# Kernel tuning notes

Measured on AMD Instinct MI355X. Metric: run time of the kernel, lower is better.

The kernel has to match this reference:

```python
import jax, jax.numpy as jnp
import numpy as np

N_NODES = 50000
N_EDGES = 800000
N_GRAPHS = 256
W_SCALE = 0.05  # keep activations bounded through 5 relu conv layers


def setup_inputs() -> dict:
    key = jax.random.key(0)
    ks = jax.random.split(key, 16)
    rn = lambda k, shape: W_SCALE * jax.random.normal(k, shape, dtype=jnp.float32)
    return {
        "x": jax.random.normal(ks[0], (N_NODES, 336), dtype=jnp.float32),
        "edge_index": jax.random.randint(ks[1], (2, N_EDGES), 0, N_NODES, dtype=jnp.int32),
        "batch": jnp.sort(jax.random.randint(ks[2], (N_NODES,), 0, N_GRAPHS, dtype=jnp.int32)),
        "w1_rel": rn(ks[3], (100, 336)),
        "w1_root": rn(ks[4], (100, 336)),
        "b1": rn(ks[5], (100,)),
        "w_rel": rn(ks[6], (4, 100, 100)),
        "w_root": rn(ks[7], (4, 100, 100)),
        "b": rn(ks[8], (4, 100)),
        "lw1": rn(ks[9], (100, 100)),
        "lb1": rn(ks[10], (100,)),
        "lw2": rn(ks[11], (100, 100)),
        "lb2": rn(ks[12], (100,)),
        "lw3": rn(ks[13], (29, 100)),
        "lb3": rn(ks[14], (29,)),
    }


def _graph_conv(x, edge_index, w_rel, w_root, bias):
    # PyG GraphConv: out_i = W_rel @ (sum_{j->i} x_j) + b + W_root @ x_i
    src, dst = edge_index[0], edge_index[1]
    agg = jax.ops.segment_sum(x[src], dst, num_segments=x.shape[0])  # [N, d_in]
    return agg @ w_rel.T + bias + x @ w_root.T


def reference(x, edge_index, batch, w1_rel, w1_root, b1, w_rel, w_root, b,
              lw1, lb1, lw2, lb2, lw3, lb3):
    h = jax.nn.relu(_graph_conv(x, edge_index, w1_rel, w1_root, b1))  # [N,100]
    for i in range(4):  # conv2..conv5 (structurally distinct params)
        h = jax.nn.relu(_graph_conv(h, edge_index, w_rel[i], w_root[i], b[i]))
    # global_mean_pool over graphs
    sums = jax.ops.segment_sum(h, batch, num_segments=N_GRAPHS)          # [G,100]
    counts = jax.ops.segment_sum(jnp.ones((h.shape[0],), h.dtype), batch,
                                 num_segments=N_GRAPHS)                  # [G]
    pooled = sums / jnp.maximum(counts, 1.0)[:, None]
    h = jax.nn.relu(pooled @ lw1.T + lb1)
    h = jax.nn.relu(h @ lw2.T + lb2)
    return h @ lw3.T + lb3  # [G, 29]
```

## Files before the change

### kernel.cpp

```cpp
#include <hip/hip_runtime.h>

#define N_NODES 50000
#define N_EDGES 800000
#define N_GRAPHS 256
#define F 100

#define SCAN_B 512
#define SCAN_NB 98
#define SCAN_PAD (SCAN_NB * SCAN_B)

#define PART_SZ 6250
#define FILL_CHUNK 2048

#define SROW 72

typedef __attribute__((ext_vector_type(8))) short bf16x8;
typedef __attribute__((ext_vector_type(4))) float f32x4;
typedef unsigned short ushort_t;
typedef unsigned int uint_t;

__device__ inline ushort_t f2bf(float f) {
  uint_t u = __float_as_uint(f);
  uint_t r = (u + 0x7fffu + ((u >> 16) & 1u)) >> 16;
  return (ushort_t)r;
}


__global__ __launch_bounds__(256) void hist_kernel(const int* __restrict__ dst,
                                                   int* __restrict__ cnt, int E) {
  int part = blockIdx.x & 7;
  int lo = part * PART_SZ, hi = lo + PART_SZ;
  int base = (blockIdx.x >> 3) * FILL_CHUNK;
  int end = base + FILL_CHUNK; if (end > E) end = E;
  for (int i = base + threadIdx.x; i < end; i += 256) {
    int d = dst[i];
    if (d >= lo && d < hi) atomicAdd(&cnt[d], 1);
  }
}

__global__ __launch_bounds__(SCAN_B) void scan1_kernel(const int* __restrict__ cnt,
                                                       int* __restrict__ excl,
                                                       int* __restrict__ bsum) {
  __shared__ int sh[SCAN_B];
  int t = threadIdx.x;
  int i = blockIdx.x * SCAN_B + t;
  int v = cnt[i];
  sh[t] = v;
  __syncthreads();
  for (int off = 1; off < SCAN_B; off <<= 1) {
    int u = (t >= off) ? sh[t - off] : 0;
    __syncthreads();
    sh[t] += u;
    __syncthreads();
  }
  excl[i] = sh[t] - v;
  if (t == SCAN_B - 1) bsum[blockIdx.x] = sh[t];
}

__global__ __launch_bounds__(128) void scan2_kernel(int* __restrict__ bsum) {
  __shared__ int sh[128];
  int t = threadIdx.x;
  int v = (t < SCAN_NB) ? bsum[t] : 0;
  sh[t] = v;
  __syncthreads();
  for (int off = 1; off < 128; off <<= 1) {
    int u = (t >= off) ? sh[t - off] : 0;
    __syncthreads();
    sh[t] += u;
    __syncthreads();
  }
  if (t < SCAN_NB) bsum[t] = sh[t] - v;
}

__global__ __launch_bounds__(SCAN_B) void scan3_kernel(const int* __restrict__ excl,
                                                       const int* __restrict__ bsum,
                                                       int* __restrict__ offs,
                                                       int* __restrict__ cursor) {
  int i = blockIdx.x * SCAN_B + threadIdx.x;
  int v = excl[i] + bsum[blockIdx.x];
  if (i <= N_NODES) { offs[i] = v; cursor[i] = v; }
}

__global__ __launch_bounds__(256) void fill_kernel(const int* __restrict__ src,
                                                   const int* __restrict__ dst,
                                                   int* __restrict__ cursor,
                                                   int* __restrict__ csr_src, int E) {
  int part = blockIdx.x & 7;
  int lo = part * PART_SZ, hi = lo + PART_SZ;
  int base = (blockIdx.x >> 3) * FILL_CHUNK;
  int end = base + FILL_CHUNK; if (end > E) end = E;
  for (int i = base + threadIdx.x; i < end; i += 256) {
    int d = dst[i];
    if (d >= lo && d < hi) {
      int p = atomicAdd(&cursor[d], 1);
      csr_src[p] = src[i];
    }
  }
}


__global__ void pack_w1_kernel(const float* __restrict__ w1_rel, const float* __restrict__ w1_root,
                               ushort_t* __restrict__ Wp1) {
  int row = blockIdx.x;
  for (int k = threadIdx.x; k < 384; k += 128) {
    float v = 0.f;
    if (k < 336) {
      if (row < 100) v = w1_rel[row * 336 + k];
      else if (row < 200) v = w1_root[(row - 100) * 336 + k];
    }
    Wp1[(size_t)row * 384 + k] = f2bf(v);
  }
}

__global__ void pack_w_kernel(const float* __restrict__ w_rel, const float* __restrict__ w_root,
                              ushort_t* __restrict__ Wp) {
  int row = blockIdx.x;
  int l = blockIdx.y;
  int k = threadIdx.x;
  float v = 0.f;
  if (k < 100) {
    if (row < 100) v = w_rel[((size_t)l * 100 + row) * 100 + k];
    else if (row < 200) v = w_root[((size_t)l * 100 + row - 100) * 100 + k];
  }
  Wp[((size_t)l * 208 + row) * 128 + k] = f2bf(v);
}


template <bool AF32>
__global__ __launch_bounds__(256) void conv_mfma(
    const void* __restrict__ Aptr, const ushort_t* __restrict__ Wp,
    const float* __restrict__ bias,
    ushort_t* __restrict__ Zrel, ushort_t* __restrict__ Zroot, int Kp) {
  __shared__ short alds[64 * SROW];
  __shared__ short blds[208 * SROW];
  __shared__ float bias_s[104];

  int tid = threadIdx.x;
  int n0 = blockIdx.x * 64;
  if (tid < 100) bias_s[tid] = bias[tid];

  f32x4 acc[13];
#pragma unroll
  for (int b = 0; b < 13; ++b) acc[b] = (f32x4)0.f;

  int w = tid >> 6, lane = tid & 63, q = lane >> 4, m16 = lane & 15;

  int ar[2], aq[2];
#pragma unroll
  for (int u = 0; u < 2; ++u) { int c = tid + u * 256; ar[u] = c >> 3; aq[u] = c & 7; }

  bf16x8 areg[2], breg[7];

  auto load_chunk = [&](int k0) {
#pragma unroll
    for (int u = 0; u < 2; ++u) {
      int node = n0 + ar[u];
      int k = k0 + aq[u] * 8;
      bf16x8 val = (bf16x8)0;
      if (AF32) {
        if (node < N_NODES && k < 336) {
          const float* p = (const float*)Aptr + (size_t)node * 336 + k;
          float4 f0 = *(const float4*)p;
          float4 f1 = *(const float4*)(p + 4);
          val[0] = (short)f2bf(f0.x); val[1] = (short)f2bf(f0.y);
          val[2] = (short)f2bf(f0.z); val[3] = (short)f2bf(f0.w);
          val[4] = (short)f2bf(f1.x); val[5] = (short)f2bf(f1.y);
          val[6] = (short)f2bf(f1.z); val[7] = (short)f2bf(f1.w);
        }
      } else {
        if (node < N_NODES)
          val = *(const bf16x8*)((const short*)Aptr + (size_t)node * 128 + k);
      }
      areg[u] = val;
    }
#pragma unroll
    for (int u = 0; u < 7; ++u) {
      int c = tid + u * 256;
      if (c < 1664) {
        int r = c >> 3, qq = c & 7;
        breg[u] = *(const bf16x8*)((const short*)Wp + (size_t)r * Kp + k0 + qq * 8);
      }
    }
  };

  load_chunk(0);

  for (int k0 = 0; k0 < Kp; k0 += 64) {
#pragma unroll
    for (int u = 0; u < 2; ++u)
      *(bf16x8*)&alds[ar[u] * SROW + aq[u] * 8] = areg[u];
#pragma unroll
    for (int u = 0; u < 7; ++u) {
      int c = tid + u * 256;
      if (c < 1664) {
        int r = c >> 3, qq = c & 7;
        *(bf16x8*)&blds[r * SROW + qq * 8] = breg[u];
      }
    }
    __syncthreads();
    if (k0 + 64 < Kp) load_chunk(k0 + 64);
#pragma unroll
    for (int s = 0; s < 2; ++s) {
      bf16x8 a = *(const bf16x8*)&alds[(w * 16 + m16) * SROW + s * 32 + q * 8];
#pragma unroll
      for (int b = 0; b < 13; ++b) {
        bf16x8 bf = *(const bf16x8*)&blds[(b * 16 + m16) * SROW + s * 32 + q * 8];
        acc[b] = __builtin_amdgcn_mfma_f32_16x16x32_bf16(a, bf, acc[b], 0, 0, 0);
      }
    }
    __syncthreads();
  }

  int node_base = n0 + w * 16 + q * 4;
#pragma unroll
  for (int b = 0; b < 13; ++b) {
    int n = b * 16 + m16;
#pragma unroll
    for (int r = 0; r < 4; ++r) {
      int node = node_base + r;
      if (node >= N_NODES) continue;
      float v = acc[b][r];
      if (n < 100) {
        Zrel[(size_t)node * 100 + n] = f2bf(v);
      } else if (n < 200) {
        Zroot[(size_t)node * 100 + (n - 100)] = f2bf(v + bias_s[n - 100]);
      }
    }
  }
}


__global__ __launch_bounds__(256) void gather_bf16(
    const ushort_t* __restrict__ Zrel, const ushort_t* __restrict__ Zroot,
    const int* __restrict__ offs, const int* __restrict__ csr,
    ushort_t* __restrict__ H) {
  int node = blockIdx.x * 4 + (threadIdx.x >> 6);
  node = __builtin_amdgcn_readfirstlane(node);
  int lane = threadIdx.x & 63;
  int off = (lane < 50 ? lane : 49) * 2;

  uint_t z = *(const uint_t*)(Zroot + (size_t)node * 100 + off);
  float p0[8], p1[8];
#pragma unroll
  for (int u = 0; u < 8; ++u) { p0[u] = 0.f; p1[u] = 0.f; }
  p0[0] = __uint_as_float(z << 16);
  p1[0] = __uint_as_float(z & 0xffff0000u);

  int s = offs[node], e = offs[node + 1];
  for (int j = s; j < e; j += 64) {
    int take = e - j; if (take > 64) take = 64;
    int vidx = (lane < take) ? csr[j + lane] : 0;
    int u = 0;
    for (; u + 8 <= take; u += 8) {
      uint_t zz[8];
#pragma unroll
      for (int t = 0; t < 8; ++t) {
        int idx = __builtin_amdgcn_readlane(vidx, u + t);
        zz[t] = *(const uint_t*)(Zrel + (size_t)idx * 100 + off);
      }
#pragma unroll
      for (int t = 0; t < 8; ++t) {
        p0[t] += __uint_as_float(zz[t] << 16);
        p1[t] += __uint_as_float(zz[t] & 0xffff0000u);
      }
    }
    int cnt = take - u;
    if (cnt > 0) {
      uint_t zz[7];
#pragma unroll
      for (int t = 0; t < 7; ++t) {
        if (t < cnt) {
          int idx = __builtin_amdgcn_readlane(vidx, u + t);
          zz[t] = *(const uint_t*)(Zrel + (size_t)idx * 100 + off);
        }
      }
#pragma unroll
      for (int t = 0; t < 7; ++t) {
        if (t < cnt) {
          p0[t] += __uint_as_float(zz[t] << 16);
          p1[t] += __uint_as_float(zz[t] & 0xffff0000u);
        }
      }
    }
  }
  float a0 = ((p0[0] + p0[1]) + (p0[2] + p0[3])) + ((p0[4] + p0[5]) + (p0[6] + p0[7]));
  float a1 = ((p1[0] + p1[1]) + (p1[2] + p1[3])) + ((p1[4] + p1[5]) + (p1[6] + p1[7]));
  a0 = fmaxf(a0, 0.f);
  a1 = fmaxf(a1, 0.f);
  uint_t outp = (uint_t)f2bf(a0) | ((uint_t)f2bf(a1) << 16);
  if (lane >= 50) outp = 0u;
  *(uint_t*)(H + (size_t)node * 128 + lane * 2) = outp;
}


__global__ __launch_bounds__(1024) void pool_kernel(const ushort_t* __restrict__ H,
                                                    const int* __restrict__ batch,
                                                    float* __restrict__ pooled) {
  int g = blockIdx.x;
  int t = threadIdx.x;
  int lo = 0, hi = N_NODES;
  while (lo < hi) { int mid = (lo + hi) >> 1; if (batch[mid] < g) lo = mid + 1; else hi = mid; }
  int s = lo;
  hi = N_NODES;
  while (lo < hi) { int mid = (lo + hi) >> 1; if (batch[mid] <= g) lo = mid + 1; else hi = mid; }
  int e = lo;

  int row = t >> 6;
  int lane = t & 63;
  int off = (lane < 50 ? lane : 49) * 2;
  float a0 = 0.f, a1 = 0.f;
  for (int n = s + row; n < e; n += 16) {
    uint_t z = *(const uint_t*)(H + (size_t)n * 128 + off);
    a0 += __uint_as_float(z << 16);
    a1 += __uint_as_float(z & 0xffff0000u);
  }
  __shared__ float sh[16][104];
  if (lane < 50) { sh[row][lane * 2] = a0; sh[row][lane * 2 + 1] = a1; }
  __syncthreads();
  if (t < 100) {
    float acc = 0.f;
#pragma unroll
    for (int r = 0; r < 16; ++r) acc += sh[r][t];
    int cnt = e - s;
    float d = (cnt > 0) ? (float)cnt : 1.f;
    pooled[(size_t)g * F + t] = acc / d;
  }
}


__global__ void mlp_kernel(const float* __restrict__ pooled,
                           const float* __restrict__ lw1, const float* __restrict__ lb1,
                           const float* __restrict__ lw2, const float* __restrict__ lb2,
                           const float* __restrict__ lw3, const float* __restrict__ lb3,
                           float* __restrict__ out) {
  int g = blockIdx.x;
  int t = threadIdx.x;
  __shared__ float r0[F], r1[F], r2[F];
  if (t < F) r0[t] = pooled[(size_t)g * F + t];
  __syncthreads();
  if (t < F) {
    float s = lb1[t];
    for (int k = 0; k < F; ++k) s += r0[k] * lw1[t * F + k];
    r1[t] = fmaxf(s, 0.f);
  }
  __syncthreads();
  if (t < F) {
    float s = lb2[t];
    for (int k = 0; k < F; ++k) s += r1[k] * lw2[t * F + k];
    r2[t] = fmaxf(s, 0.f);
  }
  __syncthreads();
  if (t < 29) {
    float s = lb3[t];
    for (int k = 0; k < F; ++k) s += r2[k] * lw3[t * F + k];
    out[g * 29 + t] = s;
  }
}


extern "C" void kernel_launch(void* const* d_in, const int* in_sizes, int n_in,
                              void* d_out, int out_size, void* d_ws, size_t ws_size,
                              hipStream_t stream) {
  const float* x       = (const float*)d_in[0];
  const int*   ei      = (const int*)d_in[1];
  const int*   batch   = (const int*)d_in[2];
  const float* w1_rel  = (const float*)d_in[3];
  const float* w1_root = (const float*)d_in[4];
  const float* b1      = (const float*)d_in[5];
  const float* w_rel   = (const float*)d_in[6];
  const float* w_root  = (const float*)d_in[7];
  const float* bvec    = (const float*)d_in[8];
  const float* lw1     = (const float*)d_in[9];
  const float* lb1     = (const float*)d_in[10];
  const float* lw2     = (const float*)d_in[11];
  const float* lb2     = (const float*)d_in[12];
  const float* lw3     = (const float*)d_in[13];
  const float* lb3     = (const float*)d_in[14];
  float* out = (float*)d_out;

  char* ws = (char*)d_ws;
  size_t o = 0;
  auto alloc = [&](size_t bytes) { void* p = ws + o; o = (o + bytes + 511) & ~(size_t)511; return p; };
  ushort_t* H    = (ushort_t*)alloc((size_t)N_NODES * 128 * 2);
  ushort_t* Zrel = (ushort_t*)alloc((size_t)N_NODES * 100 * 2);
  ushort_t* Zroot= (ushort_t*)alloc((size_t)N_NODES * 100 * 2);
  ushort_t* Wp1  = (ushort_t*)alloc((size_t)208 * 384 * 2);
  ushort_t* Wp   = (ushort_t*)alloc((size_t)4 * 208 * 128 * 2);
  float*    pooled = (float*)alloc((size_t)N_GRAPHS * F * 4);
  int* cnt    = (int*)alloc((size_t)SCAN_PAD * 4);
  int* excl   = (int*)alloc((size_t)SCAN_PAD * 4);
  int* bsum   = (int*)alloc((size_t)128 * 4);
  int* offs   = (int*)alloc((size_t)(N_NODES + 1) * 4);
  int* cursor = (int*)alloc((size_t)(N_NODES + 1) * 4);
  int* csr    = (int*)alloc((size_t)N_EDGES * 4);

  const int E = N_EDGES;
  const int* srcv = ei;
  const int* dstv = ei + E;

  int nchunk = (E + FILL_CHUNK - 1) / FILL_CHUNK;
  hipMemsetAsync(cnt, 0, (size_t)SCAN_PAD * sizeof(int), stream);
  hist_kernel<<<nchunk * 8, 256, 0, stream>>>(dstv, cnt, E);
  scan1_kernel<<<SCAN_NB, SCAN_B, 0, stream>>>(cnt, excl, bsum);
  scan2_kernel<<<1, 128, 0, stream>>>(bsum);
  scan3_kernel<<<SCAN_NB, SCAN_B, 0, stream>>>(excl, bsum, offs, cursor);
  fill_kernel<<<nchunk * 8, 256, 0, stream>>>(srcv, dstv, cursor, csr, E);

  pack_w1_kernel<<<208, 128, 0, stream>>>(w1_rel, w1_root, Wp1);
  pack_w_kernel<<<dim3(208, 4), 128, 0, stream>>>(w_rel, w_root, Wp);

  int mmgrid = (N_NODES + 63) / 64;
  conv_mfma<true><<<mmgrid, 256, 0, stream>>>(x, Wp1, b1, Zrel, Zroot, 384);
  gather_bf16<<<N_NODES / 4, 256, 0, stream>>>(Zrel, Zroot, offs, csr, H);
  for (int l = 0; l < 4; ++l) {
    conv_mfma<false><<<mmgrid, 256, 0, stream>>>(H, Wp + (size_t)l * 208 * 128,
                                                 bvec + (size_t)l * F, Zrel, Zroot, 128);
    gather_bf16<<<N_NODES / 4, 256, 0, stream>>>(Zrel, Zroot, offs, csr, H);
  }
  pool_kernel<<<N_GRAPHS, 1024, 0, stream>>>(H, batch, pooled);
  mlp_kernel<<<N_GRAPHS, 128, 0, stream>>>(pooled, lw1, lb1, lw2, lb2, lw3, lb3, out);
}
```

Baseline: 458.6 us.

## Interleave Zrel/Zroot into padded rows and stage epilogue through LDS

Merges the two per-node projection outputs into one padded 256-element bf16 row per node (rel at 0, root at 128) and writes it from the GEMM epilogue via shared memory with 16-byte coalesced stores instead of scattered 2-byte stores. The gather kernel then reads rel and root from the aligned padded rows. This targets uncoalesced epilogue writes and misaligned 200-byte row strides. In exchange it writes more bytes per node because of the padding, and the gathered rel half-rows sit at a wider stride, which could reduce cache density in the gather.

```diff
diff --git a/kernel.cpp b/kernel.cpp
--- a/kernel.cpp
+++ b/kernel.cpp
@@ -13,6 +13,7 @@
 #define FILL_CHUNK 2048
 
 #define SROW 72
+#define EPS 264
 
 typedef __attribute__((ext_vector_type(8))) short bf16x8;
 typedef __attribute__((ext_vector_type(4))) float f32x4;
@@ -130,10 +131,11 @@
 __global__ __launch_bounds__(256) void conv_mfma(
     const void* __restrict__ Aptr, const ushort_t* __restrict__ Wp,
     const float* __restrict__ bias,
-    ushort_t* __restrict__ Zrel, ushort_t* __restrict__ Zroot, int Kp) {
-  __shared__ short alds[64 * SROW];
-  __shared__ short blds[208 * SROW];
+    ushort_t* __restrict__ ZP, int Kp) {
+  __shared__ short smem[64 * SROW + 208 * SROW];
   __shared__ float bias_s[104];
+  short* alds = smem;
+  short* blds = smem + 64 * SROW;
 
   int tid = threadIdx.x;
   int n0 = blockIdx.x * 64;
@@ -211,27 +213,36 @@
     __syncthreads();
   }
 
-  int node_base = n0 + w * 16 + q * 4;
+  short* ep = smem;
 #pragma unroll
   for (int b = 0; b < 13; ++b) {
     int n = b * 16 + m16;
-#pragma unroll
-    for (int r = 0; r < 4; ++r) {
-      int node = node_base + r;
-      if (node >= N_NODES) continue;
-      float v = acc[b][r];
-      if (n < 100) {
-        Zrel[(size_t)node * 100 + n] = f2bf(v);
-      } else if (n < 200) {
-        Zroot[(size_t)node * 100 + (n - 100)] = f2bf(v + bias_s[n - 100]);
-      }
+    if (n < 200) {
+      int c = (n < 100) ? n : (n + 28);
+      float add = (n < 100) ? 0.f : bias_s[(n - 100) & 127];
+#pragma unroll
+      for (int r = 0; r < 4; ++r) {
+        int row = w * 16 + q * 4 + r;
+        ep[row * EPS + c] = (short)f2bf(acc[b][r] + add);
+      }
+    }
+  }
+  __syncthreads();
+#pragma unroll
+  for (int j = 0; j < 8; ++j) {
+    int i = tid + j * 256;
+    int row = i >> 5, c16 = i & 31;
+    int node = n0 + row;
+    if (node < N_NODES) {
+      *(uint4*)(ZP + (size_t)node * 256 + c16 * 8) =
+          *(const uint4*)&ep[row * EPS + c16 * 8];
     }
   }
 }
 
 
 __global__ __launch_bounds__(256) void gather_bf16(
-    const ushort_t* __restrict__ Zrel, const ushort_t* __restrict__ Zroot,
+    const ushort_t* __restrict__ ZP,
     const int* __restrict__ offs, const int* __restrict__ csr,
     ushort_t* __restrict__ H) {
   int node = blockIdx.x * 4 + (threadIdx.x >> 6);
@@ -239,7 +250,7 @@
   int lane = threadIdx.x & 63;
   int off = (lane < 50 ? lane : 49) * 2;
 
-  uint_t z = *(const uint_t*)(Zroot + (size_t)node * 100 + off);
+  uint_t z = *(const uint_t*)(ZP + (size_t)node * 256 + 128 + off);
   float p0[8], p1[8];
 #pragma unroll
   for (int u = 0; u < 8; ++u) { p0[u] = 0.f; p1[u] = 0.f; }
@@ -256,7 +267,7 @@
 #pragma unroll
       for (int t = 0; t < 8; ++t) {
         int idx = __builtin_amdgcn_readlane(vidx, u + t);
-        zz[t] = *(const uint_t*)(Zrel + (size_t)idx * 100 + off);
+        zz[t] = *(const uint_t*)(ZP + (size_t)idx * 256 + off);
       }
 #pragma unroll
       for (int t = 0; t < 8; ++t) {
@@ -271,7 +282,7 @@
       for (int t = 0; t < 7; ++t) {
         if (t < cnt) {
           int idx = __builtin_amdgcn_readlane(vidx, u + t);
-          zz[t] = *(const uint_t*)(Zrel + (size_t)idx * 100 + off);
+          zz[t] = *(const uint_t*)(ZP + (size_t)idx * 256 + off);
         }
       }
 #pragma unroll
@@ -382,8 +393,7 @@
   size_t o = 0;
   auto alloc = [&](size_t bytes) { void* p = ws + o; o = (o + bytes + 511) & ~(size_t)511; return p; };
   ushort_t* H    = (ushort_t*)alloc((size_t)N_NODES * 128 * 2);
-  ushort_t* Zrel = (ushort_t*)alloc((size_t)N_NODES * 100 * 2);
-  ushort_t* Zroot= (ushort_t*)alloc((size_t)N_NODES * 100 * 2);
+  ushort_t* ZP   = (ushort_t*)alloc((size_t)N_NODES * 256 * 2);
   ushort_t* Wp1  = (ushort_t*)alloc((size_t)208 * 384 * 2);
   ushort_t* Wp   = (ushort_t*)alloc((size_t)4 * 208 * 128 * 2);
   float*    pooled = (float*)alloc((size_t)N_GRAPHS * F * 4);
@@ -410,12 +420,12 @@
   pack_w_kernel<<<dim3(208, 4), 128, 0, stream>>>(w_rel, w_root, Wp);
 
   int mmgrid = (N_NODES + 63) / 64;
-  conv_mfma<true><<<mmgrid, 256, 0, stream>>>(x, Wp1, b1, Zrel, Zroot, 384);
-  gather_bf16<<<N_NODES / 4, 256, 0, stream>>>(Zrel, Zroot, offs, csr, H);
+  conv_mfma<true><<<mmgrid, 256, 0, stream>>>(x, Wp1, b1, ZP, 384);
+  gather_bf16<<<N_NODES / 4, 256, 0, stream>>>(ZP, offs, csr, H);
   for (int l = 0; l < 4; ++l) {
     conv_mfma<false><<<mmgrid, 256, 0, stream>>>(H, Wp + (size_t)l * 208 * 128,
-                                                 bvec + (size_t)l * F, Zrel, Zroot, 128);
-    gather_bf16<<<N_NODES / 4, 256, 0, stream>>>(Zrel, Zroot, offs, csr, H);
+                                                 bvec + (size_t)l * F, ZP, 128);
+    gather_bf16<<<N_NODES / 4, 256, 0, stream>>>(ZP, offs, csr, H);
   }
   pool_kernel<<<N_GRAPHS, 1024, 0, stream>>>(H, batch, pooled);
   mlp_kernel<<<N_GRAPHS, 128, 0, stream>>>(pooled, lw1, lb1, lw2, lb2, lw3, lb3, out);
```

Measured after the change: 456.7 us. About the same (-0.4%).
